# Kernel tuning notes

Hardware: AMD Instinct MI355X
Metric: run time of the kernel (lower is better)

## Reference

```python
import jax, jax.numpy as jnp
import numpy as np

T, B, D = 2048, 4, 1024


def setup_inputs() -> dict:
    key = jax.random.key(0)
    ks = jax.random.split(key, 4)
    data = jax.random.normal(ks[0], (T, B, D), dtype=jnp.float32)
    W_qkv = jax.random.normal(ks[1], (D, 3 * D), dtype=jnp.float32) * 0.02
    b_qkv = jnp.zeros((3 * D,), dtype=jnp.float32)
    # torch stores pos_bias as [1,1,T,T]; bilinear interp to the same [T,T] size
    # (align_corners=False) is the identity, so we keep a [T,T] table directly.
    pos_bias_param = jax.random.normal(ks[2], (T, T), dtype=jnp.float32) * 0.02
    W_out = jax.random.normal(ks[3], (D, D), dtype=jnp.float32) * 0.02
    b_out = jnp.zeros((D,), dtype=jnp.float32)
    return {"data": data, "W_qkv": W_qkv, "b_qkv": b_qkv,
            "pos_bias_param": pos_bias_param, "W_out": W_out, "b_out": b_out}


def reference(data, W_qkv, b_qkv, pos_bias_param, W_out, b_out):
    # data: [T, B, D]
    qkv = data @ W_qkv + b_qkv                      # [T, B, 3D]
    q, k, v = jnp.split(qkv, 3, axis=-1)            # each [T, B, D]
    pb = pos_bias_param                             # [T, T] (i=query pos, j=key pos)
    max_key = jnp.max(k, axis=0, keepdims=True)     # [1, B, D]
    max_pb = jnp.max(pb, axis=1, keepdims=True)     # [T, 1]
    exp_key = jnp.exp(k - max_key)                  # [T, B, D]
    exp_pb = jnp.exp(pb - max_pb)                   # [T, T]
    # torch einsum 'ijb,jbd->ibd' with b=1 on pos_bias broadcasts -> plain ij contraction
    num = jnp.einsum('ij,jbd->ibd', exp_pb, exp_key * v)  # [T, B, D]
    den = jnp.einsum('ij,jbd->ibd', exp_pb, exp_key)       # [T, B, D]
    y = jax.nn.sigmoid(q) * num / den               # [T, B, D]
    return y @ W_out + b_out
```

## Files before the change

### kernel.cpp

```cpp
#include <hip/hip_runtime.h>
#include <stdint.h>

typedef unsigned short ushort_t;
typedef signed char s8;
typedef __attribute__((ext_vector_type(8))) short short8;
typedef __attribute__((ext_vector_type(4))) int int4v;
typedef __attribute__((ext_vector_type(4))) float float4v;

typedef const void __attribute__((address_space(1)))* gptr1_t;
typedef void __attribute__((address_space(3)))* lptr3_t;

#define SX   (5.5f/127.f)
#define ISX  (127.f/5.5f)
#define SW1  (0.11f/127.f)
#define ISW1 (127.f/0.11f)
#define S1   (SX*SW1)

static __device__ __forceinline__ ushort_t f2bf(float f) {
  unsigned u = __builtin_bit_cast(unsigned, f);
  u += 0x7fffu + ((u >> 16) & 1u);
  return (ushort_t)(u >> 16);
}
static __device__ __forceinline__ float bf2f(ushort_t h) {
  unsigned u = ((unsigned)h) << 16;
  return __builtin_bit_cast(float, u);
}
static __device__ __forceinline__ float frcp(float x) { return __builtin_amdgcn_rcpf(x); }
static __device__ __forceinline__ int q8(float x, float inv_s) {
  float v = fminf(fmaxf(x * inv_s, -127.f), 127.f);
  return (int)rintf(v);
}

__global__ __launch_bounds__(256)
void prep1(const float* __restrict__ data, s8* __restrict__ Xq,
           const float* __restrict__ Wqkv, s8* __restrict__ WqT) {
  __shared__ float t[32][33];
  const int blk = blockIdx.x, tid = threadIdx.x;
  if (blk < 8192) {
    int row = blk;
    int orow = (row & 3) * 2048 + (row >> 2);
    float4v v = ((const float4v*)(data + (size_t)row * 1024))[tid];
    int a0 = q8(v[0], ISX), a1 = q8(v[1], ISX), a2 = q8(v[2], ISX), a3 = q8(v[3], ISX);
    uint32_t p = (a0 & 255) | ((a1 & 255) << 8) | ((a2 & 255) << 16) | ((a3 & 255) << 24);
    ((uint32_t*)(Xq + (size_t)orow * 1024))[tid] = p;
  } else {
    int l = blk - 8192;
    int bx = l % 96, by = l / 96;
    int tx = tid & 31, ty = tid >> 5;
    int c = bx * 32 + tx;
    #pragma unroll
    for (int i = ty; i < 32; i += 8)
      t[i][tx] = Wqkv[(size_t)(by * 32 + i) * 3072 + c];
    __syncthreads();
    int r = by * 32 + tx;
    #pragma unroll
    for (int i = ty; i < 32; i += 8) {
      int orow = bx * 32 + i;
      orow = (orow < 1024) ? orow
           : (orow < 2048) ? 1024 + 2 * (orow - 1024)
                           : 1024 + 2 * (orow - 2048) + 1;
      WqT[(size_t)orow * 1024 + r] = (s8)q8(t[tx][i], ISW1);
    }
  }
}


#define FENCE() asm volatile("" ::: "memory")
#define BARRIER() do { FENCE(); __builtin_amdgcn_s_barrier(); FENCE(); } while (0)
#define WAIT_LGKM0() do { asm volatile("s_waitcnt lgkmcnt(0)" ::: "memory"); \
                          __builtin_amdgcn_sched_barrier(0); } while (0)
#define WAIT_VM4() do { asm volatile("s_waitcnt vmcnt(4)" ::: "memory"); \
                        __builtin_amdgcn_sched_barrier(0); } while (0)
#define WAIT_VM0() do { asm volatile("s_waitcnt vmcnt(0)" ::: "memory"); \
                        __builtin_amdgcn_sched_barrier(0); } while (0)

#define GLD(g, l) __builtin_amdgcn_global_load_lds((gptr1_t)(const void*)(g), \
                                                   (lptr3_t)(void*)(l), 16, 0, 0)

#define STAGEA(h, u, bb) do { \
  const char* gs_ = gA + (size_t)(h) * 128 * AROWB + (size_t)(u) * 128; \
  char* ls_ = Als + (bb) * 32768 + (((h) * 128 + wid * 16) << 7); \
  GLD(gs_, ls_); GLD(gs_ + 8 * AROWB, ls_ + 1024); \
} while (0)
#define STAGEB(h, u, bb) do { \
  const char* gs_ = gB + (size_t)(h) * 128 * BROWB + (size_t)(u) * 128; \
  char* ls_ = Bls + (bb) * 32768 + (((h) * 128 + wid * 16) << 7); \
  GLD(gs_, ls_); GLD(gs_ + 8 * BROWB, ls_ + 1024); \
} while (0)

#define LDA4(ih, bb) do { \
  const fragt* As_ = (const fragt*)(Als + (bb) * 32768); \
  _Pragma("unroll") \
  for (int ii_ = 0; ii_ < 4; ++ii_) { \
    const int row_ = wr * 128 + ((ih) * 4 + ii_) * 16 + m16; \
    af[ii_][0] = As_[row_ * 8 + (quad ^ swr)]; \
    af[ii_][1] = As_[row_ * 8 + ((4 + quad) ^ swr)]; \
  } \
} while (0)

#define LDB2(jh, bb) do { \
  const fragt* Bs_ = (const fragt*)(Bls + (bb) * 32768); \
  _Pragma("unroll") \
  for (int jj_ = 0; jj_ < 2; ++jj_) { \
    const int row_ = wc * 64 + ((jh) * 2 + jj_) * 16 + m16; \
    bf[(jh) * 2 + jj_][0] = Bs_[row_ * 8 + (quad ^ swr)]; \
    bf[(jh) * 2 + jj_][1] = Bs_[row_ * 8 + ((4 + quad) ^ swr)]; \
  } \
} while (0)

#define MM16(ih, jh) do { \
  __builtin_amdgcn_s_setprio(1); \
  _Pragma("unroll") \
  for (int ks_ = 0; ks_ < 2; ++ks_) \
    _Pragma("unroll") \
    for (int ii_ = 0; ii_ < 4; ++ii_) \
      _Pragma("unroll") \
      for (int jj_ = 0; jj_ < 2; ++jj_) \
        acc[(ih) * 4 + ii_][(jh) * 2 + jj_] = MFMA_OP( \
            af[ii_][ks_], bf[(jh) * 2 + jj_][ks_], acc[(ih) * 4 + ii_][(jh) * 2 + jj_]); \
  __builtin_amdgcn_s_setprio(0); \
  __builtin_amdgcn_sched_barrier(0); \
} while (0)

#define GROUP4(bb, tA, tB) do { \
  LDA4(0, bb); LDB2(0, bb); STAGEA(0, tA, (bb) ^ 1); STAGEA(1, tA, (bb) ^ 1); \
  BARRIER(); WAIT_LGKM0(); MM16(0, 0); BARRIER(); \
  LDB2(1, bb); \
  BARRIER(); WAIT_LGKM0(); MM16(0, 1); BARRIER(); \
  LDA4(1, bb); STAGEB(0, tB, bb); STAGEB(1, tB, bb); \
  BARRIER(); WAIT_LGKM0(); MM16(1, 0); BARRIER(); \
  WAIT_VM4(); \
  BARRIER(); WAIT_LGKM0(); MM16(1, 1); BARRIER(); \
} while (0)

#define GROUP4_A(bb, tA) do { \
  LDA4(0, bb); LDB2(0, bb); STAGEA(0, tA, (bb) ^ 1); STAGEA(1, tA, (bb) ^ 1); \
  BARRIER(); WAIT_LGKM0(); MM16(0, 0); BARRIER(); \
  LDB2(1, bb); \
  BARRIER(); WAIT_LGKM0(); MM16(0, 1); BARRIER(); \
  LDA4(1, bb); \
  BARRIER(); WAIT_LGKM0(); MM16(1, 0); BARRIER(); \
  WAIT_VM0(); \
  BARRIER(); WAIT_LGKM0(); MM16(1, 1); BARRIER(); \
} while (0)

#define GROUP4_N(bb) do { \
  LDA4(0, bb); LDB2(0, bb); \
  BARRIER(); WAIT_LGKM0(); MM16(0, 0); BARRIER(); \
  LDB2(1, bb); \
  BARRIER(); WAIT_LGKM0(); MM16(0, 1); BARRIER(); \
  LDA4(1, bb); \
  BARRIER(); WAIT_LGKM0(); MM16(1, 0); BARRIER(); \
  BARRIER(); WAIT_LGKM0(); MM16(1, 1); \
} while (0)

#define MFMA_OP(a, b, c) __builtin_amdgcn_mfma_i32_16x16x64_i8(a, b, c, 0, 0, 0)
__global__ __launch_bounds__(512, 2)
void g1mix(const s8* __restrict__ WqT, const s8* __restrict__ Xq,
           const float* __restrict__ bqkv,
           uint32_t* __restrict__ qP, ushort_t* __restrict__ GT,
           const float* __restrict__ pb, ushort_t* __restrict__ Pb,
           const float* __restrict__ Wout, ushort_t* __restrict__ WoT) {
  __shared__ __align__(16) char smem[131072];
  const int blk = blockIdx.x, tid = threadIdx.x;
  if (blk < 384) {
    typedef int4v fragt;
    const int wid  = tid >> 6;
    const int lane = tid & 63;
    const int wr = wid >> 2, wc = wid & 3;
    const int m16 = lane & 15, quad = lane >> 4;
    const int swr = m16 & 7;
    const int srow = lane >> 3, schk = lane & 7;

    const int wg = (blk & 7) * 48 + (blk >> 3);
    const int m0 = (wg >> 5) * 256;
    const int n0 = (wg & 31) * 256;

    int4v acc[8][4];
    #pragma unroll
    for (int i = 0; i < 8; ++i)
      #pragma unroll
      for (int j = 0; j < 4; ++j)
        #pragma unroll
        for (int r = 0; r < 4; ++r) acc[i][j][r] = 0;

    fragt af[4][2], bf[4][2];

    const size_t AROWB = 1024, BROWB = 1024;
    const int colb = (schk ^ srow) * 16;
    const char* gA = (const char*)WqT + (size_t)(m0 + wid * 16 + srow) * 1024 + colb;
    const char* gB = (const char*)Xq  + (size_t)(n0 + wid * 16 + srow) * 1024 + colb;
    char* Als = smem;
    char* Bls = smem + 65536;

    STAGEA(0, 0, 0); STAGEA(1, 0, 0);
    STAGEB(0, 0, 0); STAGEB(1, 0, 0);
    STAGEB(0, 1, 1); STAGEB(1, 1, 1);
    WAIT_VM4();
    BARRIER();

    #pragma unroll 1
    for (int I = 0; I < 3; ++I) {
      GROUP4(0, 2 * I + 1, 2 * I + 2);
      GROUP4(1, 2 * I + 2, 2 * I + 3);
    }
    GROUP4_A(0, 7);
    GROUP4_N(1);

    if (m0 < 1024) {
      #pragma unroll
      for (int i = 0; i < 8; ++i)
        #pragma unroll
        for (int j = 0; j < 4; ++j) {
          const int gm = m0 + wr * 128 + i * 16 + quad * 4;
          const int gn = n0 + wc * 64 + j * 16 + m16;
          float f0 = (float)acc[i][j][0] * S1 + bqkv[gm];
          float f1 = (float)acc[i][j][1] * S1 + bqkv[gm + 1];
          float f2 = (float)acc[i][j][2] * S1 + bqkv[gm + 2];
          float f3 = (float)acc[i][j][3] * S1 + bqkv[gm + 3];
          qP[(size_t)(gm >> 1) * 8192 + gn]       = (uint32_t)f2bf(f0) | ((uint32_t)f2bf(f1) << 16);
          qP[(size_t)((gm >> 1) + 1) * 8192 + gn] = (uint32_t)f2bf(f2) | ((uint32_t)f2bf(f3) << 16);
        }
    } else {
      #pragma unroll
      for (int i = 0; i < 8; ++i)
        #pragma unroll
        for (int j = 0; j < 4; ++j) {
          const int gm = m0 + wr * 128 + i * 16 + quad * 4;
          const int gn = n0 + wc * 64 + j * 16 + m16;
          const int d  = (gm - 1024) >> 1;
          const int t  = gn & 2047, bb = gn >> 11;
          #pragma unroll
          for (int p = 0; p < 2; ++p) {
            float kk = (float)acc[i][j][2 * p]     * S1 + bqkv[1024 + d + p];
            float vv = (float)acc[i][j][2 * p + 1] * S1 + bqkv[2048 + d + p];
            float ek = __expf(kk);
            int c = bb * 1024 + d + p;
            GT[(size_t)(2 * c)     * 2048 + t] = f2bf(ek * vv);
            GT[(size_t)(2 * c + 1) * 2048 + t] = f2bf(ek);
          }
        }
    }
  } else if (blk < 640) {
    const int base = (blk - 384) * 4096;
    #pragma unroll
    for (int r = 0; r < 8; ++r) {
      int i = base + r * 512 + tid;
      float4v v = *(const float4v*)(pb + (size_t)i * 4);
      ushort_t o0 = f2bf(__expf(v[0])), o1 = f2bf(__expf(v[1]));
      ushort_t o2 = f2bf(__expf(v[2])), o3 = f2bf(__expf(v[3]));
      uint64_t p = (uint64_t)o0 | ((uint64_t)o1 << 16) | ((uint64_t)o2 << 32) | ((uint64_t)o3 << 48);
      *(uint64_t*)(Pb + (size_t)i * 4) = p;
    }
  } else {
    float (*t)[33] = (float (*)[33])smem;
    const int tx = tid & 31, ty = tid >> 5;
    #pragma unroll 1
    for (int rep = 0; rep < 8; ++rep) {
      int l = (blk - 640) * 8 + rep;
      int bx = l & 31, by = l >> 5;
      int c = bx * 32 + tx;
      #pragma unroll
      for (int i = ty; i < 32; i += 16)
        t[i][tx] = Wout[(size_t)(by * 32 + i) * 1024 + c];
      __syncthreads();
      int r = by * 32 + tx;
      #pragma unroll
      for (int i = ty; i < 32; i += 16)
        WoT[(size_t)(bx * 32 + i) * 1024 + r] = f2bf(t[tx][i]);
      __syncthreads();
    }
  }
}
#undef MFMA_OP

template <int K>
__global__ __launch_bounds__(256)
void gemm_bt(const ushort_t* __restrict__ A, const ushort_t* __restrict__ BT,
             const float* __restrict__ bias, float* __restrict__ Cf, int M, int N) {
  __shared__ __align__(16) char smem[32768];
  short8* As = (short8*)smem;
  short8* Bs = As + 1024;
  const int tid  = threadIdx.x;
  const int wid  = tid >> 6;
  const int lane = tid & 63;
  const int wr = wid >> 1, wc = wid & 1;
  const int m16 = lane & 15, quad = lane >> 4;

  const int n0 = blockIdx.x * 128;
  const int m0 = blockIdx.y * 128;

  float4v acc[4][4];
  #pragma unroll
  for (int i = 0; i < 4; ++i)
    #pragma unroll
    for (int j = 0; j < 4; ++j)
      #pragma unroll
      for (int r = 0; r < 4; ++r) acc[i][j][r] = 0.0f;

  const int srow = lane >> 3, schk = lane & 7;
  const ushort_t* pa[4];
  const ushort_t* pb[4];
  #pragma unroll
  for (int g = 0; g < 4; ++g) {
    int rl = wid * 32 + g * 8 + srow;
    int cg = schk ^ (rl & 7);
    pa[g] = A  + (size_t)(m0 + rl) * K + cg * 8;
    pb[g] = BT + (size_t)(n0 + rl) * K + cg * 8;
  }
  const int swr = m16 & 7;

  #pragma unroll 1
  for (int k0 = 0; k0 < K; k0 += 64) {
    __syncthreads();
    #pragma unroll
    for (int g = 0; g < 4; ++g) {
      GLD(pa[g], As + (wid * 32 + g * 8) * 8);
      GLD(pb[g], Bs + (wid * 32 + g * 8) * 8);
      pa[g] += 64; pb[g] += 64;
    }
    __syncthreads();

    #pragma unroll
    for (int ks = 0; ks < 2; ++ks) {
      const int chk = (ks * 4 + quad) ^ swr;
      short8 af[4], bfr[4];
      #pragma unroll
      for (int i = 0; i < 4; ++i)
        af[i] = As[(wr * 64 + i * 16 + m16) * 8 + chk];
      #pragma unroll
      for (int j = 0; j < 4; ++j)
        bfr[j] = Bs[(wc * 64 + j * 16 + m16) * 8 + chk];
      #pragma unroll
      for (int i = 0; i < 4; ++i)
        #pragma unroll
        for (int j = 0; j < 4; ++j)
          acc[i][j] = __builtin_amdgcn_mfma_f32_16x16x32_bf16(af[i], bfr[j], acc[i][j], 0, 0, 0);
    }
  }

  #pragma unroll
  for (int i = 0; i < 4; ++i)
    #pragma unroll
    for (int j = 0; j < 4; ++j) {
      const int gm = m0 + wr * 64 + i * 16 + quad * 4;
      const int gn = n0 + wc * 64 + j * 16 + m16;
      const float bv = bias[gn];
      #pragma unroll
      for (int r = 0; r < 4; ++r)
        Cf[(size_t)(gm + r) * N + gn] = acc[i][j][r] + bv;
    }
}

#define MFMA_OP(a, b, c) __builtin_amdgcn_mfma_f32_16x16x32_bf16(a, b, c, 0, 0, 0)
__global__ __launch_bounds__(512, 2)
void aft256(const ushort_t* __restrict__ A, const ushort_t* __restrict__ BT,
            ushort_t* __restrict__ Yb, const uint32_t* __restrict__ qP) {
  __shared__ __align__(16) char smem[131072];
  typedef short8 fragt;
  const int tid  = threadIdx.x;
  const int wid  = tid >> 6;
  const int lane = tid & 63;
  const int wr = wid >> 2, wc = wid & 3;
  const int m16 = lane & 15, quad = lane >> 4;
  const int swr = m16 & 7;
  const int srow = lane >> 3, schk = lane & 7;

  const int bid = blockIdx.x;
  const int wg = (bid & 7) * 32 + (bid >> 3);
  const int m0 = (wg >> 3) * 256;
  const int n0 = (wg & 7) * 256;

  float4v acc[8][4];
  #pragma unroll
  for (int i = 0; i < 8; ++i)
    #pragma unroll
    for (int j = 0; j < 4; ++j)
      #pragma unroll
      for (int r = 0; r < 4; ++r) acc[i][j][r] = 0.0f;

  fragt af[4][2], bf[4][2];

  const size_t AROWB = 4096, BROWB = 4096;
  const int colb = (schk ^ srow) * 16;
  const char* gA = (const char*)A  + (size_t)(m0 + wid * 16 + srow) * 4096 + colb;
  const char* gB = (const char*)BT + (size_t)(n0 + wid * 16 + srow) * 4096 + colb;
  char* Als = smem;
  char* Bls = smem + 65536;

  STAGEA(0, 0, 0); STAGEA(1, 0, 0);
  STAGEB(0, 0, 0); STAGEB(1, 0, 0);
  STAGEB(0, 1, 1); STAGEB(1, 1, 1);
  WAIT_VM4();
  BARRIER();

  #pragma unroll 1
  for (int I = 0; I < 15; ++I) {
    GROUP4(0, 2 * I + 1, 2 * I + 2);
    GROUP4(1, 2 * I + 2, 2 * I + 3);
  }
  GROUP4_A(0, 31);
  GROUP4_N(1);

  __syncthreads();

  uint32_t* tb = (uint32_t*)smem;
  const int cbase = m0 >> 1;
  const int b = cbase >> 10, dbase = cbase & 1023;
  const int pbase = dbase >> 1;
  #pragma unroll
  for (int i = 0; i < 8; ++i) {
    const int wl = wr * 32 + i * 4 + quad;
    #pragma unroll
    for (int j = 0; j < 4; ++j) {
      const int tl = wc * 64 + j * 16 + m16;
      const int t  = n0 + tl;
      uint32_t qw = qP[(size_t)(pbase + wl) * 8192 + b * 2048 + t];
      float q0 = bf2f((ushort_t)(qw & 0xffffu));
      float q1 = bf2f((ushort_t)(qw >> 16));
      float y0 = frcp(1.0f + __expf(-q0)) * acc[i][j][0] * frcp(acc[i][j][1]);
      float y1 = frcp(1.0f + __expf(-q1)) * acc[i][j][2] * frcp(acc[i][j][3]);
      tb[tl * 65 + wl] = (uint32_t)f2bf(y0) | ((uint32_t)f2bf(y1) << 16);
    }
  }
  __syncthreads();
  uint32_t* Yw = (uint32_t*)Yb;
  const int lw = tid & 63, trow = tid >> 6;
  #pragma unroll
  for (int it = 0; it < 32; ++it) {
    const int tl = it * 8 + trow;
    const int t  = n0 + tl;
    Yw[(size_t)(4 * t + b) * 512 + (dbase >> 1) + lw] = tb[tl * 65 + lw];
  }
}
#undef MFMA_OP


extern "C" void kernel_launch(void* const* d_in, const int* in_sizes, int n_in,
                              void* d_out, int out_size, void* d_ws, size_t ws_size,
                              hipStream_t stream) {
  const float* data = (const float*)d_in[0];
  const float* Wqkv = (const float*)d_in[1];
  const float* bqkv = (const float*)d_in[2];
  const float* pb   = (const float*)d_in[3];
  const float* Wout = (const float*)d_in[4];
  const float* bout = (const float*)d_in[5];
  float* out = (float*)d_out;

  char* ws = (char*)d_ws;
  s8*       Xq  = (s8*)(ws);
  s8*       WqT = (s8*)(ws + (8ull  << 20));
  ushort_t* WoT = (ushort_t*)(ws + (11ull << 20));
  ushort_t* Pb  = (ushort_t*)(ws + (13ull << 20));
  uint32_t* qPw = (uint32_t*)(ws + (21ull << 20));
  ushort_t* GT  = (ushort_t*)(ws + (37ull << 20));
  ushort_t* Y   = (ushort_t*)(ws + (69ull << 20));

  prep1<<<11264, 256, 0, stream>>>(data, Xq, Wqkv, WqT);
  g1mix<<<768, 512, 0, stream>>>(WqT, Xq, bqkv, qPw, GT, pb, Pb, Wout, WoT);
  aft256<<<256, 512, 0, stream>>>(GT, Pb, Y, qPw);
  gemm_bt<1024><<<dim3(8, 64), 256, 0, stream>>>(Y, WoT, bout, out, 8192, 1024);
}
```

Before: 235.6 us.

## Restructure GEMM main loops into double-buffered tiles with partial lgkm waits

Replaces the old four-phase GROUP4 schedule, which had barriers around every MFMA group, with a per-tile body. Each tile prefetches the whole next K-tile of A and B into the other buffer, then interleaves LDS fragment loads and MFMAs using partial lgkmcnt waits, with a single barrier per tile. The same pipelined scheme is applied to the small gemm_bt kernel, which previously did a synchronous single-buffered load-then-compute loop. That kernel gets double-buffered LDS and launch_bounds(256,2). The aim is fewer barriers and better overlap of loads with MFMAs, at the cost of more LDS in gemm_bt and a tighter dependence on the counted waits being correct.

```diff
diff --git a/kernel.cpp b/kernel.cpp
--- a/kernel.cpp
+++ b/kernel.cpp
@@ -67,12 +67,11 @@
 
 #define FENCE() asm volatile("" ::: "memory")
 #define BARRIER() do { FENCE(); __builtin_amdgcn_s_barrier(); FENCE(); } while (0)
-#define WAIT_LGKM0() do { asm volatile("s_waitcnt lgkmcnt(0)" ::: "memory"); \
-                          __builtin_amdgcn_sched_barrier(0); } while (0)
-#define WAIT_VM4() do { asm volatile("s_waitcnt vmcnt(4)" ::: "memory"); \
-                        __builtin_amdgcn_sched_barrier(0); } while (0)
-#define WAIT_VM0() do { asm volatile("s_waitcnt vmcnt(0)" ::: "memory"); \
-                        __builtin_amdgcn_sched_barrier(0); } while (0)
+#define SB() __builtin_amdgcn_sched_barrier(0)
+#define WAIT_LGKM0() do { asm volatile("s_waitcnt lgkmcnt(0)" ::: "memory"); SB(); } while (0)
+#define WAIT_LGKM4() do { asm volatile("s_waitcnt lgkmcnt(4)" ::: "memory"); SB(); } while (0)
+#define WAIT_LGKM8() do { asm volatile("s_waitcnt lgkmcnt(8)" ::: "memory"); SB(); } while (0)
+#define WAIT_VM0()   do { asm volatile("s_waitcnt vmcnt(0)"   ::: "memory"); SB(); } while (0)
 
 #define GLD(g, l) __builtin_amdgcn_global_load_lds((gptr1_t)(const void*)(g), \
                                                    (lptr3_t)(void*)(l), 16, 0, 0)
@@ -88,71 +87,73 @@
   GLD(gs_, ls_); GLD(gs_ + 8 * BROWB, ls_ + 1024); \
 } while (0)
 
-#define LDA4(ih, bb) do { \
+#define STAGE4(gbase, lbase, tn, bb, ROWB) do { \
+  const char* gs_ = (gbase) + (size_t)(tn) * 128; \
+  char* ls_ = (lbase) + (bb) * 32768 + ((wid * 32) << 7); \
+  GLD(gs_, ls_); GLD(gs_ + 8 * (size_t)(ROWB), ls_ + 1024); \
+  GLD(gs_ + 16 * (size_t)(ROWB), ls_ + 2048); GLD(gs_ + 24 * (size_t)(ROWB), ls_ + 3072); \
+} while (0)
+
+#define LDA2(DST, p, bb) do { \
   const fragt* As_ = (const fragt*)(Als + (bb) * 32768); \
   _Pragma("unroll") \
-  for (int ii_ = 0; ii_ < 4; ++ii_) { \
-    const int row_ = wr * 128 + ((ih) * 4 + ii_) * 16 + m16; \
-    af[ii_][0] = As_[row_ * 8 + (quad ^ swr)]; \
-    af[ii_][1] = As_[row_ * 8 + ((4 + quad) ^ swr)]; \
+  for (int ii_ = 0; ii_ < 2; ++ii_) { \
+    const int row_ = arow + ((p) * 2 + ii_) * 16 + m16; \
+    DST[ii_][0] = As_[row_ * 8 + (quad ^ swr)]; \
+    DST[ii_][1] = As_[row_ * 8 + ((4 + quad) ^ swr)]; \
   } \
 } while (0)
-
-#define LDB2(jh, bb) do { \
+#define LDB2Q(DST, q, bb) do { \
   const fragt* Bs_ = (const fragt*)(Bls + (bb) * 32768); \
   _Pragma("unroll") \
   for (int jj_ = 0; jj_ < 2; ++jj_) { \
-    const int row_ = wc * 64 + ((jh) * 2 + jj_) * 16 + m16; \
-    bf[(jh) * 2 + jj_][0] = Bs_[row_ * 8 + (quad ^ swr)]; \
-    bf[(jh) * 2 + jj_][1] = Bs_[row_ * 8 + ((4 + quad) ^ swr)]; \
+    const int row_ = brow + ((q) * 2 + jj_) * 16 + m16; \
+    DST[jj_][0] = Bs_[row_ * 8 + (quad ^ swr)]; \
+    DST[jj_][1] = Bs_[row_ * 8 + ((4 + quad) ^ swr)]; \
   } \
 } while (0)
 
-#define MM16(ih, jh) do { \
+#define MM8(AF, BF, ib, jb) do { \
   __builtin_amdgcn_s_setprio(1); \
   _Pragma("unroll") \
   for (int ks_ = 0; ks_ < 2; ++ks_) \
     _Pragma("unroll") \
-    for (int ii_ = 0; ii_ < 4; ++ii_) \
+    for (int ii_ = 0; ii_ < 2; ++ii_) \
       _Pragma("unroll") \
       for (int jj_ = 0; jj_ < 2; ++jj_) \
-        acc[(ih) * 4 + ii_][(jh) * 2 + jj_] = MFMA_OP( \
-            af[ii_][ks_], bf[(jh) * 2 + jj_][ks_], acc[(ih) * 4 + ii_][(jh) * 2 + jj_]); \
+        acc[(ib) + ii_][(jb) + jj_] = MFMA_OP( \
+            AF[ii_][ks_], BF[jj_][ks_], acc[(ib) + ii_][(jb) + jj_]); \
   __builtin_amdgcn_s_setprio(0); \
-  __builtin_amdgcn_sched_barrier(0); \
-} while (0)
-
-#define GROUP4(bb, tA, tB) do { \
-  LDA4(0, bb); LDB2(0, bb); STAGEA(0, tA, (bb) ^ 1); STAGEA(1, tA, (bb) ^ 1); \
-  BARRIER(); WAIT_LGKM0(); MM16(0, 0); BARRIER(); \
-  LDB2(1, bb); \
-  BARRIER(); WAIT_LGKM0(); MM16(0, 1); BARRIER(); \
-  LDA4(1, bb); STAGEB(0, tB, bb); STAGEB(1, tB, bb); \
-  BARRIER(); WAIT_LGKM0(); MM16(1, 0); BARRIER(); \
-  WAIT_VM4(); \
-  BARRIER(); WAIT_LGKM0(); MM16(1, 1); BARRIER(); \
-} while (0)
-
-#define GROUP4_A(bb, tA) do { \
-  LDA4(0, bb); LDB2(0, bb); STAGEA(0, tA, (bb) ^ 1); STAGEA(1, tA, (bb) ^ 1); \
-  BARRIER(); WAIT_LGKM0(); MM16(0, 0); BARRIER(); \
-  LDB2(1, bb); \
-  BARRIER(); WAIT_LGKM0(); MM16(0, 1); BARRIER(); \
-  LDA4(1, bb); \
-  BARRIER(); WAIT_LGKM0(); MM16(1, 0); BARRIER(); \
+  SB(); \
+} while (0)
+
+#define TILE256_BODY(bb) \
+  LDA2(afX, 0, bb); LDB2Q(bfQ0, 0, bb); SB(); \
+  LDA2(afY, 1, bb); LDB2Q(bfQ1, 1, bb); SB(); \
+  WAIT_LGKM8(); \
+  MM8(afX, bfQ0, 0, 0); \
+  WAIT_LGKM0(); \
+  MM8(afX, bfQ1, 0, 2); \
+  LDA2(afX, 2, bb); SB(); \
+  MM8(afY, bfQ0, 2, 0); \
+  MM8(afY, bfQ1, 2, 2); \
+  LDA2(afY, 3, bb); SB(); \
+  WAIT_LGKM4(); \
+  MM8(afX, bfQ0, 4, 0); \
+  MM8(afX, bfQ1, 4, 2); \
+  WAIT_LGKM0(); \
+  MM8(afY, bfQ0, 6, 0); \
+  MM8(afY, bfQ1, 6, 2);
+
+#define TILE256(bb, tn) do { \
+  STAGEA(0, tn, (bb) ^ 1); STAGEA(1, tn, (bb) ^ 1); \
+  STAGEB(0, tn, (bb) ^ 1); STAGEB(1, tn, (bb) ^ 1); \
+  TILE256_BODY(bb) \
   WAIT_VM0(); \
-  BARRIER(); WAIT_LGKM0(); MM16(1, 1); BARRIER(); \
-} while (0)
-
-#define GROUP4_N(bb) do { \
-  LDA4(0, bb); LDB2(0, bb); \
-  BARRIER(); WAIT_LGKM0(); MM16(0, 0); BARRIER(); \
-  LDB2(1, bb); \
-  BARRIER(); WAIT_LGKM0(); MM16(0, 1); BARRIER(); \
-  LDA4(1, bb); \
-  BARRIER(); WAIT_LGKM0(); MM16(1, 0); BARRIER(); \
-  BARRIER(); WAIT_LGKM0(); MM16(1, 1); \
-} while (0)
+  BARRIER(); \
+} while (0)
+
+#define TILE256_LAST(bb) do { TILE256_BODY(bb) } while (0)
 
 #define MFMA_OP(a, b, c) __builtin_amdgcn_mfma_i32_16x16x64_i8(a, b, c, 0, 0, 0)
 __global__ __launch_bounds__(512, 2)
@@ -171,6 +172,7 @@
     const int m16 = lane & 15, quad = lane >> 4;
     const int swr = m16 & 7;
     const int srow = lane >> 3, schk = lane & 7;
+    const int arow = wr * 128, brow = wc * 64;
 
     const int wg = (blk & 7) * 48 + (blk >> 3);
     const int m0 = (wg >> 5) * 256;
@@ -184,7 +186,7 @@
         #pragma unroll
         for (int r = 0; r < 4; ++r) acc[i][j][r] = 0;
 
-    fragt af[4][2], bf[4][2];
+    fragt afX[2][2], afY[2][2], bfQ0[2][2], bfQ1[2][2];
 
     const size_t AROWB = 1024, BROWB = 1024;
     const int colb = (schk ^ srow) * 16;
@@ -193,19 +195,17 @@
     char* Als = smem;
     char* Bls = smem + 65536;
 
-    STAGEA(0, 0, 0); STAGEA(1, 0, 0);
-    STAGEB(0, 0, 0); STAGEB(1, 0, 0);
-    STAGEB(0, 1, 1); STAGEB(1, 1, 1);
-    WAIT_VM4();
+    STAGEA(0, 0, 0); STAGEA(1, 0, 0); STAGEB(0, 0, 0); STAGEB(1, 0, 0);
+    WAIT_VM0();
     BARRIER();
 
     #pragma unroll 1
     for (int I = 0; I < 3; ++I) {
-      GROUP4(0, 2 * I + 1, 2 * I + 2);
-      GROUP4(1, 2 * I + 2, 2 * I + 3);
-    }
-    GROUP4_A(0, 7);
-    GROUP4_N(1);
+      TILE256(0, 2 * I + 1);
+      TILE256(1, 2 * I + 2);
+    }
+    TILE256(0, 7);
+    TILE256_LAST(1);
 
     if (m0 < 1024) {
       #pragma unroll
@@ -274,18 +274,41 @@
 }
 #undef MFMA_OP
 
+#define MFMA_OP(a, b, c) __builtin_amdgcn_mfma_f32_16x16x32_bf16(a, b, c, 0, 0, 0)
+#define TILE128_BODY(bb) \
+  LDA2(afX, 0, bb); LDB2Q(bfQ0, 0, bb); SB(); \
+  LDA2(afY, 1, bb); LDB2Q(bfQ1, 1, bb); SB(); \
+  WAIT_LGKM8(); \
+  MM8(afX, bfQ0, 0, 0); \
+  WAIT_LGKM0(); \
+  MM8(afX, bfQ1, 0, 2); \
+  MM8(afY, bfQ0, 2, 0); \
+  MM8(afY, bfQ1, 2, 2);
+
+#define TILE128(bb, tn) do { \
+  STAGE4(gA, Als, tn, (bb) ^ 1, 2048); \
+  STAGE4(gB, Bls, tn, (bb) ^ 1, 2048); \
+  TILE128_BODY(bb) \
+  WAIT_VM0(); \
+  BARRIER(); \
+} while (0)
+
+#define TILE128_LAST(bb) do { TILE128_BODY(bb) } while (0)
+
 template <int K>
-__global__ __launch_bounds__(256)
+__global__ __launch_bounds__(256, 2)
 void gemm_bt(const ushort_t* __restrict__ A, const ushort_t* __restrict__ BT,
              const float* __restrict__ bias, float* __restrict__ Cf, int M, int N) {
-  __shared__ __align__(16) char smem[32768];
-  short8* As = (short8*)smem;
-  short8* Bs = As + 1024;
+  __shared__ __align__(16) char smem[65536];
+  typedef short8 fragt;
   const int tid  = threadIdx.x;
   const int wid  = tid >> 6;
   const int lane = tid & 63;
   const int wr = wid >> 1, wc = wid & 1;
   const int m16 = lane & 15, quad = lane >> 4;
+  const int swr = m16 & 7;
+  const int srow = lane >> 3, schk = lane & 7;
+  const int arow = wr * 64, brow = wc * 64;
 
   const int n0 = blockIdx.x * 128;
   const int m0 = blockIdx.y * 128;
@@ -298,46 +321,26 @@
       #pragma unroll
       for (int r = 0; r < 4; ++r) acc[i][j][r] = 0.0f;
 
-  const int srow = lane >> 3, schk = lane & 7;
-  const ushort_t* pa[4];
-  const ushort_t* pb[4];
-  #pragma unroll
-  for (int g = 0; g < 4; ++g) {
-    int rl = wid * 32 + g * 8 + srow;
-    int cg = schk ^ (rl & 7);
-    pa[g] = A  + (size_t)(m0 + rl) * K + cg * 8;
-    pb[g] = BT + (size_t)(n0 + rl) * K + cg * 8;
-  }
-  const int swr = m16 & 7;
+  fragt afX[2][2], afY[2][2], bfQ0[2][2], bfQ1[2][2];
+
+  const int colb = (schk ^ srow) * 16;
+  const char* gA = (const char*)A  + (size_t)(m0 + wid * 32 + srow) * (K * 2) + colb;
+  const char* gB = (const char*)BT + (size_t)(n0 + wid * 32 + srow) * (K * 2) + colb;
+  char* Als = smem;
+  char* Bls = smem + 16384;
+
+  STAGE4(gA, Als, 0, 0, 2048);
+  STAGE4(gB, Bls, 0, 0, 2048);
+  WAIT_VM0();
+  BARRIER();
 
   #pragma unroll 1
-  for (int k0 = 0; k0 < K; k0 += 64) {
-    __syncthreads();
-    #pragma unroll
-    for (int g = 0; g < 4; ++g) {
-      GLD(pa[g], As + (wid * 32 + g * 8) * 8);
-      GLD(pb[g], Bs + (wid * 32 + g * 8) * 8);
-      pa[g] += 64; pb[g] += 64;
-    }
-    __syncthreads();
-
-    #pragma unroll
-    for (int ks = 0; ks < 2; ++ks) {
-      const int chk = (ks * 4 + quad) ^ swr;
-      short8 af[4], bfr[4];
-      #pragma unroll
-      for (int i = 0; i < 4; ++i)
-        af[i] = As[(wr * 64 + i * 16 + m16) * 8 + chk];
-      #pragma unroll
-      for (int j = 0; j < 4; ++j)
-        bfr[j] = Bs[(wc * 64 + j * 16 + m16) * 8 + chk];
-      #pragma unroll
-      for (int i = 0; i < 4; ++i)
-        #pragma unroll
-        for (int j = 0; j < 4; ++j)
-          acc[i][j] = __builtin_amdgcn_mfma_f32_16x16x32_bf16(af[i], bfr[j], acc[i][j], 0, 0, 0);
-    }
-  }
+  for (int I = 0; I < 7; ++I) {
+    TILE128(0, 2 * I + 1);
+    TILE128(1, 2 * I + 2);
+  }
+  TILE128(0, 15);
+  TILE128_LAST(1);
 
   #pragma unroll
   for (int i = 0; i < 4; ++i)
@@ -351,6 +354,7 @@
         Cf[(size_t)(gm + r) * N + gn] = acc[i][j][r] + bv;
     }
 }
+#undef MFMA_OP
 
 #define MFMA_OP(a, b, c) __builtin_amdgcn_mfma_f32_16x16x32_bf16(a, b, c, 0, 0, 0)
 __global__ __launch_bounds__(512, 2)
@@ -365,6 +369,7 @@
   const int m16 = lane & 15, quad = lane >> 4;
   const int swr = m16 & 7;
   const int srow = lane >> 3, schk = lane & 7;
+  const int arow = wr * 128, brow = wc * 64;
 
   const int bid = blockIdx.x;
   const int wg = (bid & 7) * 32 + (bid >> 3);
@@ -379,7 +384,7 @@
       #pragma unroll
       for (int r = 0; r < 4; ++r) acc[i][j][r] = 0.0f;
 
-  fragt af[4][2], bf[4][2];
+  fragt afX[2][2], afY[2][2], bfQ0[2][2], bfQ1[2][2];
 
   const size_t AROWB = 4096, BROWB = 4096;
   const int colb = (schk ^ srow) * 16;
@@ -388,19 +393,17 @@
   char* Als = smem;
   char* Bls = smem + 65536;
 
-  STAGEA(0, 0, 0); STAGEA(1, 0, 0);
-  STAGEB(0, 0, 0); STAGEB(1, 0, 0);
-  STAGEB(0, 1, 1); STAGEB(1, 1, 1);
-  WAIT_VM4();
+  STAGEA(0, 0, 0); STAGEA(1, 0, 0); STAGEB(0, 0, 0); STAGEB(1, 0, 0);
+  WAIT_VM0();
   BARRIER();
 
   #pragma unroll 1
   for (int I = 0; I < 15; ++I) {
-    GROUP4(0, 2 * I + 1, 2 * I + 2);
-    GROUP4(1, 2 * I + 2, 2 * I + 3);
-  }
-  GROUP4_A(0, 31);
-  GROUP4_N(1);
+    TILE256(0, 2 * I + 1);
+    TILE256(1, 2 * I + 2);
+  }
+  TILE256(0, 31);
+  TILE256_LAST(1);
 
   __syncthreads();
 
```

Result: faster. 230.5 us (-2.2%).
